# Performance work log

Hardware: AMD Instinct MI355X
Metric: run time of the kernel (lower is better)

## Reference

```python
import jax, jax.numpy as jnp
import numpy as np

EPS = 1e-5

def knn_idx(x, k):
    # x: (B,C,N). Returns (B,N,k) indices of k nearest neighbors (by L2).
    inner = -2.0 * jnp.einsum('bcn,bcm->bnm', x, x)          # (B,N,N)
    xx = jnp.sum(x * x, axis=1)                               # (B,N)
    neg_dist = -xx[:, :, None] - inner - xx[:, None, :]       # (B,N,N)
    _, idx = jax.lax.top_k(neg_dist, k)                       # (B,N,k)
    return idx

def get_graph_features(x, k):
    # x: (B,C,N) -> (B,2C,N,k) with channels = concat(neighbor-center, center)
    B, C, N = x.shape
    idx = knn_idx(x, k)                                       # (B,N,k)
    pts = jnp.transpose(x, (0, 2, 1))                         # (B,N,C)
    nbr = jax.vmap(lambda p, i: p[i])(pts, idx)               # (B,N,k,C)
    ctr = jnp.broadcast_to(pts[:, :, None, :], nbr.shape)     # (B,N,k,C)
    feat = jnp.concatenate([nbr - ctr, ctr], axis=-1)         # (B,N,k,2C)
    return jnp.transpose(feat, (0, 3, 1, 2))                  # (B,2C,N,k)

def conv_bn_relu(y, W, gamma, beta):
    # 1x1 conv (pointwise matmul) + train-mode BatchNorm2d + ReLU
    y = jnp.einsum('oc,bcnk->bonk', W, y)
    mean = jnp.mean(y, axis=(0, 2, 3), keepdims=True)
    var = jnp.var(y, axis=(0, 2, 3), keepdims=True)
    yhat = (y - mean) * jax.lax.rsqrt(var + EPS)
    return jax.nn.relu(yhat * gamma[None, :, None, None] + beta[None, :, None, None])

def setup_inputs() -> dict:
    key = jax.random.key(0)
    ks = jax.random.split(key, 16)
    B, N, k, emb = 8, 2048, 20, 512
    x = jax.random.normal(ks[0], (B, 3, N), dtype=jnp.float32)
    def w(kk, o, c):
        return jax.random.normal(kk, (o, c), dtype=jnp.float32) * (1.0 / np.sqrt(c))
    inp = {
        'x': x, 'k': k,
        'W1': w(ks[1], 64, 6),   'W2': w(ks[2], 64, 64),
        'W3': w(ks[3], 128, 64), 'W4': w(ks[4], 256, 128),
        'W5': w(ks[5], emb, 512),
    }
    for i, c in zip(range(1, 6), [64, 64, 128, 256, emb]):
        inp[f'g{i}'] = 1.0 + 0.1 * jax.random.normal(ks[5 + i], (c,), dtype=jnp.float32)
        inp[f'b{i}'] = 0.1 * jax.random.normal(ks[10 + i], (c,), dtype=jnp.float32)
    return inp

def reference(x, W1, W2, W3, W4, W5, g1, b1, g2, b2, g3, b3, g4, b4, g5, b5, k):
    B, C, N = x.shape
    h = get_graph_features(x, k)                  # (B,6,N,k)
    h = conv_bn_relu(h, W1, g1, b1)               # (B,64,N,k)
    x1 = jnp.max(h, axis=-1, keepdims=True)
    h = conv_bn_relu(h, W2, g2, b2)               # (B,64,N,k)
    x2 = jnp.max(h, axis=-1, keepdims=True)
    h = conv_bn_relu(h, W3, g3, b3)               # (B,128,N,k)
    x3 = jnp.max(h, axis=-1, keepdims=True)
    h = conv_bn_relu(h, W4, g4, b4)               # (B,256,N,k)
    x4 = jnp.max(h, axis=-1, keepdims=True)
    cat = jnp.concatenate([x1, x2, x3, x4], axis=1)  # (B,512,N,1)
    out = conv_bn_relu(cat, W5, g5, b5)              # (B,emb,N,1)
    return out.reshape(B, -1, N)
```

## Files before the change

### kernel.cpp

```cpp
#include <hip/hip_runtime.h>
#include <hip/hip_bf16.h>

typedef __hip_bfloat16 bf16;
typedef __attribute__((ext_vector_type(8))) short short8v;
typedef __attribute__((ext_vector_type(4))) float f32x4;
typedef unsigned int uint;
typedef unsigned long long u64;

#define BATCH 8
#define NPTS 2048
#define KNN 20
#define NK (NPTS*KNN)
#define P4 (BATCH*NK)
#define BN_TOT (BATCH*NPTS)

union BU { bf16 h; unsigned short u; };
__device__ __forceinline__ unsigned short f2bf(float f){
    BU bu; bu.h = __float2bfloat16(f); return bu.u;
}
__device__ __forceinline__ float bfu2f(unsigned short u){
    return __uint_as_float(((uint)u) << 16);
}
__device__ __forceinline__ uint fenc(float f){
    uint b = __float_as_uint(f);
    return (b & 0x80000000u) ? ~b : (b | 0x80000000u);
}

__global__ void initK(float* __restrict__ shadow)
{
    int t = blockIdx.x*256 + threadIdx.x;
    if (t < 5*16*1024) shadow[t] = 0.f;
}

__global__ void cvtWS(const float* __restrict__ src, short* __restrict__ dst, int Cin)
{
    int t = blockIdx.x*256 + threadIdx.x;
    int co = t / Cin, ci = t - co*Cin;
    dst[(size_t)co*Cin + (ci ^ ((co & 7) << 3))] = (short)f2bf(src[t]);
}

__global__ __launch_bounds__(512)
void knn_kernel(const float* __restrict__ x, int* __restrict__ idx)
{
    #pragma clang fp contract(off)
    __shared__ float4 sp[NPTS];
    const int b  = blockIdx.x / (NPTS/8);
    const int nb = blockIdx.x % (NPTS/8);
    const float* xb = x + (size_t)b*3*NPTS;
    for (int i = threadIdx.x; i < NPTS; i += 512) {
        float y0 = xb[i], y1 = xb[NPTS+i], y2 = xb[2*NPTS+i];
        float4 p; p.x = y0; p.y = y1; p.z = y2;
        p.w = y0*y0 + y1*y1 + y2*y2;
        sp[i] = p;
    }
    __syncthreads();

    const int wave = threadIdx.x >> 6;
    const int lane = threadIdx.x & 63;
    const int n = nb*8 + wave;

    const float4 pn = sp[n];
    const float x0 = pn.x, x1 = pn.y, x2 = pn.z;
    const float xxn = pn.w;

    constexpr int L = 4;
    float bA[L], bB[L]; int iA[L], iB[L];
    #pragma unroll
    for (int i = 0; i < L; ++i) {
        bA[i] = -3e38f; bB[i] = -3e38f; iA[i] = 0x7fffffff; iB[i] = 0x7fffffff;
    }

    #pragma unroll
    for (int t = 0; t < NPTS/128; ++t) {
        int m0 = lane + (2*t)*64, m1 = m0 + 64;
        float4 p0 = sp[m0], p1 = sp[m1];
        float dot0 = x0*p0.x + x1*p0.y + x2*p0.z;
        float v0 = -xxn - (-2.f*dot0) - p0.w;
        float dot1 = x0*p1.x + x1*p1.y + x2*p1.z;
        float v1 = -xxn - (-2.f*dot1) - p1.w;
        int mi0 = m0, mi1 = m1;
        #pragma unroll
        for (int i = 0; i < L; ++i) {
            { bool sw = v0 > bA[i];
              float tv = sw ? bA[i] : v0; int ti = sw ? iA[i] : mi0;
              bA[i] = sw ? v0 : bA[i]; iA[i] = sw ? mi0 : iA[i]; v0 = tv; mi0 = ti; }
            { bool sw = v1 > bB[i];
              float tv = sw ? bB[i] : v1; int ti = sw ? iB[i] : mi1;
              bB[i] = sw ? v1 : bB[i]; iB[i] = sw ? mi1 : iB[i]; v1 = tv; mi1 = ti; }
        }
    }

    u64 kA[L], kB[L];
    #pragma unroll
    for (int i = 0; i < L; ++i) {
        kA[i] = ((u64)fenc(bA[i]) << 32) | (uint)(~iA[i]);
        kB[i] = ((u64)fenc(bB[i]) << 32) | (uint)(~iB[i]);
    }

    size_t obase = ((size_t)b*NPTS + n)*KNN;
    int popA = 0, popB = 0;
    #pragma unroll 1
    for (int s = 0; s < KNN; ++s) {
        bool useA = kA[0] >= kB[0];
        u64 my = useA ? kA[0] : kB[0];
        u64 g = my;
        #pragma unroll
        for (int off = 1; off < 64; off <<= 1) {
            u64 o = __shfl_xor(g, off);
            g = (o > g) ? o : g;
        }
        if (lane == 0) idx[obase + s] = (int)(~(uint)g);
        bool win = (my == g);
        bool pA = win && useA, pB = win && !useA;
        #pragma unroll
        for (int i = 0; i < L-1; ++i) {
            kA[i] = pA ? kA[i+1] : kA[i];
            kB[i] = pB ? kB[i+1] : kB[i];
        }
        kA[L-1] = pA ? 0ULL : kA[L-1];
        kB[L-1] = pB ? 0ULL : kB[L-1];
        popA += pA; popB += pB;
    }

    if (__any((popA >= L) || (popB >= L))) {
        float B[KNN]; int BI[KNN];
        #pragma unroll
        for (int i = 0; i < KNN; ++i) { B[i] = -3e38f; BI[i] = 0x7fffffff; }
        #pragma unroll 1
        for (int j = 0; j < NPTS/64; ++j) {
            int m = lane + j*64;
            float4 p = sp[m];
            float dot = x0*p.x + x1*p.y + x2*p.z;
            float v = -xxn - (-2.f*dot) - p.w;
            int mi = m;
            #pragma unroll
            for (int i = 0; i < KNN; ++i) {
                bool sw = v > B[i];
                float tv = sw ? B[i]  : v;
                int   ti = sw ? BI[i] : mi;
                B[i]  = sw ? v  : B[i];
                BI[i] = sw ? mi : BI[i];
                v = tv; mi = ti;
            }
        }
        #pragma unroll 1
        for (int s = 0; s < KNN; ++s) {
            float mv = B[0]; int mi = BI[0];
            #pragma unroll
            for (int off = 1; off < 64; off <<= 1) {
                float ov = __shfl_xor(mv, off);
                int   oi = __shfl_xor(mi, off);
                if (ov > mv || (ov == mv && oi < mi)) { mv = ov; mi = oi; }
            }
            bool win = (B[0] == mv) && (BI[0] == mi);
            #pragma unroll
            for (int i = 0; i < KNN-1; ++i) {
                B[i]  = win ? B[i+1]  : B[i];
                BI[i] = win ? BI[i+1] : BI[i];
            }
            B[KNN-1]  = win ? -3e38f     : B[KNN-1];
            BI[KNN-1] = win ? 0x7fffffff : BI[KNN-1];
            if (lane == 0) idx[obase + s] = mi;
        }
    }
}

__global__ void conv1T(const float* __restrict__ x, const int* __restrict__ idx,
                       const float* __restrict__ W1, bf16* __restrict__ h1)
{
    int p = blockIdx.x*256 + threadIdx.x;
    int b = p / NK;
    int r = p - b*NK;
    int n = r / KNN;
    int j = idx[p];
    const float* xb = x + (size_t)b*3*NPTS;
    float c0 = xb[n], c1 = xb[NPTS+n], c2 = xb[2*NPTS+n];
    float d0 = xb[j]-c0, d1 = xb[NPTS+j]-c1, d2 = xb[2*NPTS+j]-c2;
    uint4* outp = reinterpret_cast<uint4*>(reinterpret_cast<unsigned short*>(h1) + (size_t)p*64);
    #pragma unroll
    for (int ch = 0; ch < 8; ++ch) {
        uint u[4];
        #pragma unroll
        for (int q = 0; q < 4; ++q) {
            const float* wa = W1 + (ch*8 + q*2)*6;
            float a0 = wa[0]*d0 + wa[1]*d1 + wa[2]*d2 + wa[3]*c0 + wa[4]*c1 + wa[5]*c2;
            const float* wb = wa + 6;
            float a1 = wb[0]*d0 + wb[1]*d1 + wb[2]*d2 + wb[3]*c0 + wb[4]*c1 + wb[5]*c2;
            u[q] = (uint)f2bf(a0) | ((uint)f2bf(a1) << 16);
        }
        outp[ch] = make_uint4(u[0], u[1], u[2], u[3]);
    }
}

__global__ void statsT64(const bf16* __restrict__ h, float* __restrict__ shadow)
{
    __shared__ float ls[4][64], lq[4][64];
    int t = threadIdx.x;
    int c = t & 63, grp = t >> 6;
    const unsigned short* hp = reinterpret_cast<const unsigned short*>(h);
    size_t base = (size_t)blockIdx.x*1024;
    float s = 0.f, q = 0.f;
    for (int it = 0; it < 256; ++it) {
        size_t br = base + grp + (size_t)it*4;
        float v = bfu2f(hp[br*64 + c]);
        s += v; q += v*v;
    }
    ls[grp][c] = s; lq[grp][c] = q;
    __syncthreads();
    if (t < 64) {
        float S = ls[0][t]+ls[1][t]+ls[2][t]+ls[3][t];
        float Q = lq[0][t]+lq[1][t]+lq[2][t]+lq[3][t];
        float* sh = shadow + (size_t)(blockIdx.x & 15)*1024;
        atomicAdd(&sh[t], S);
        atomicAdd(&sh[512 + t], Q);
    }
}

__global__ void fin_kernel(const float* __restrict__ shadow,
                           const float* __restrict__ gamma, const float* __restrict__ beta,
                           float* __restrict__ scbiF, int C, float invCnt)
{
    for (int c = threadIdx.x; c < C; c += 256) {
        float s = 0.f, q = 0.f;
        #pragma unroll
        for (int i = 0; i < 16; ++i) { s += shadow[i*1024 + c]; q += shadow[i*1024 + 512 + c]; }
        float m = s*invCnt;
        float var = q*invCnt - m*m;
        float rs = rsqrtf(var + 1e-5f);
        float sc = rs * gamma[c];
        float bi = fmaf(-m, sc, beta[c]);
        scbiF[2*c] = sc; scbiF[2*c+1] = bi;
    }
}

template<int Cout, int Cin, int M, int POOL, int NSPLIT, int KTILE, int BT, int PF>
__global__ __launch_bounds__(BT)
void gemmT(const short* __restrict__ Wb, const bf16* __restrict__ in,
           bf16* __restrict__ outT, float* __restrict__ shadow,
           float* __restrict__ pmax, float* __restrict__ pmin)
{
    constexpr int CSPL = Cout/NSPLIT;
    constexpr int NT   = CSPL/16;
    constexpr int ROWS = (BT/64)*16*M;
    constexpr int KSTOT = Cin/32;
    constexpr int KPT   = KTILE/32;
    constexpr int NTILE = Cin/KTILE;
    constexpr size_t WB = (size_t)CSPL*KTILE*2;
    constexpr size_t PB = POOL ? (size_t)2*ROWS*17*4 : 0;
    constexpr size_t SB = WB > PB ? WB : PB;

    __shared__ __align__(16) char smem[SB];
    short* WsmS = reinterpret_cast<short*>(smem);
    float* poolF = reinterpret_cast<float*>(smem);

    const int tid  = threadIdx.x;
    const int lane = tid & 63;
    const int g = lane >> 4, mr = lane & 15;
    const int wid = tid >> 6;
    const int rowBlk = blockIdx.x*ROWS;
    const int rowW   = rowBlk + wid*(16*M);
    const int ntBase = blockIdx.y*CSPL;
    const short* inS = reinterpret_cast<const short*>(in);

    f32x4 acc[M][NT];
    #pragma unroll
    for (int m = 0; m < M; ++m)
    #pragma unroll
    for (int i = 0; i < NT; ++i) acc[m][i] = (f32x4){0.f,0.f,0.f,0.f};

    short8v a[M], anext[M];
    if (PF) {
        #pragma unroll
        for (int m = 0; m < M; ++m)
            a[m] = *reinterpret_cast<const short8v*>(inS + (size_t)(rowW + m*16 + mr)*Cin + 8*g);
    }

    #pragma unroll 1
    for (int kt = 0; kt < NTILE; ++kt) {
        if (kt) __syncthreads();
        {
            const int ktBase = kt*KTILE;
            for (int f8 = tid; f8 < CSPL*KTILE/8; f8 += BT) {
                int f = f8*8;
                int row = f / KTILE, col = f - row*KTILE;
                short8v v = *reinterpret_cast<const short8v*>(
                    Wb + (size_t)(ntBase + row)*Cin + ktBase + col);
                *reinterpret_cast<short8v*>(WsmS + f) = v;
            }
        }
        __syncthreads();

        #pragma unroll
        for (int ksl = 0; ksl < KPT; ++ksl) {
            const int ksg = kt*KPT + ksl;
            const int k0 = ksg*32 + 8*g;
            if (!PF) {
                #pragma unroll
                for (int m = 0; m < M; ++m)
                    a[m] = *reinterpret_cast<const short8v*>(inS + (size_t)(rowW + m*16 + mr)*Cin + k0);
            } else if (ksg + 1 < KSTOT) {
                #pragma unroll
                for (int m = 0; m < M; ++m)
                    anext[m] = *reinterpret_cast<const short8v*>(inS + (size_t)(rowW + m*16 + mr)*Cin + k0 + 32);
            }
            const int kx = ksl*32 + 8*g;
            #pragma unroll
            for (int nt = 0; nt < NT; ++nt) {
                const int brow = nt*16 + mr;
                short8v bfr = *reinterpret_cast<const short8v*>(
                    WsmS + brow*KTILE + (kx ^ ((mr & 7) << 3)));
                #pragma unroll
                for (int m = 0; m < M; ++m)
                    acc[m][nt] = __builtin_amdgcn_mfma_f32_16x16x32_bf16(a[m], bfr, acc[m][nt], 0, 0, 0);
            }
            if (PF) {
                #pragma unroll
                for (int m = 0; m < M; ++m) a[m] = anext[m];
            }
        }
    }

    float* sh = shadow + (size_t)((blockIdx.x ^ blockIdx.y) & 15)*1024;
    #pragma unroll
    for (int nt = 0; nt < NT; ++nt) {
        float s = 0.f, q = 0.f;
        #pragma unroll
        for (int m = 0; m < M; ++m)
        #pragma unroll
        for (int j = 0; j < 4; ++j) { float v = acc[m][nt][j]; s += v; q += v*v; }
        s += __shfl_xor(s, 16); s += __shfl_xor(s, 32);
        q += __shfl_xor(q, 16); q += __shfl_xor(q, 32);
        if (g == 0) {
            atomicAdd(&sh[ntBase + nt*16 + mr], s);
            atomicAdd(&sh[512 + ntBase + nt*16 + mr], q);
        }
    }

    if (!POOL) {
        #pragma unroll
        for (int m = 0; m < M; ++m)
        #pragma unroll
        for (int nt = 0; nt < NT; ++nt)
        #pragma unroll
        for (int j = 0; j < 4; ++j) {
            size_t row = (size_t)rowW + m*16 + g*4 + j;
            outT[row*Cout + ntBase + nt*16 + mr] = __float2bfloat16(acc[m][nt][j]);
        }
    } else {
        __syncthreads();
        #pragma unroll
        for (int np = 0; np < NT/2; ++np) {
            #pragma unroll
            for (int hh = 0; hh < 2; ++hh) {
                #pragma unroll
                for (int m = 0; m < M; ++m)
                #pragma unroll
                for (int j = 0; j < 4; ++j) {
                    int row = wid*(16*M) + m*16 + g*4 + j;
                    poolF[hh*(ROWS*17) + row*17 + mr] = acc[m][np*2+hh][j];
                }
            }
            __syncthreads();
            if (tid < 2*(ROWS/KNN)*16) {
                int hh = tid >> 7;
                int gg = (tid >> 4) & 7;
                int cc = tid & 15;
                float mx = -3e38f, mn = 3e38f;
                #pragma unroll
                for (int kk = 0; kk < KNN; ++kk) {
                    float v = poolF[hh*(ROWS*17) + (gg*KNN + kk)*17 + cc];
                    mx = fmaxf(mx, v); mn = fminf(mn, v);
                }
                int grp = rowBlk/KNN + gg;
                int c = ntBase + (np*2 + hh)*16 + cc;
                pmax[(size_t)grp*256 + c] = mx;
                pmin[(size_t)grp*256 + c] = mn;
            }
            __syncthreads();
        }
    }
}

template<int C>
__global__ void maxpoolT(bf16* __restrict__ h, const float* __restrict__ scbiF,
                         bf16* __restrict__ catT, int coff)
{
    constexpr int PB = 256/C;
    int t = threadIdx.x;
    int c = t & (C-1);
    int bn = blockIdx.x*PB + t/C;
    float sc = scbiF[2*c], bi = scbiF[2*c+1];
    unsigned short* src = reinterpret_cast<unsigned short*>(h) + (size_t)bn*KNN*C + c;
    float best = 0.f;
    #pragma unroll
    for (int kk = 0; kk < KNN; ++kk) {
        float a = fmaxf(fmaf(bfu2f(src[kk*C]), sc, bi), 0.f);
        src[kk*C] = f2bf(a);
        best = fmaxf(best, a);
    }
    catT[(size_t)bn*512 + coff + c] = __float2bfloat16(best);
}

__global__ void cat4T(const float* __restrict__ pmax, const float* __restrict__ pmin,
                      const float* __restrict__ scbiF, const float* __restrict__ g4,
                      bf16* __restrict__ catT)
{
    int t = blockIdx.x*256 + threadIdx.x;
    int c = t & 255, bn = t >> 8;
    float sc = scbiF[2*c], bi = scbiF[2*c+1];
    float v = (g4[c] >= 0.f) ? pmax[t] : pmin[t];
    catT[(size_t)bn*512 + 256 + c] = __float2bfloat16(fmaxf(fmaf(v, sc, bi), 0.f));
}

__global__ void finalT(const bf16* __restrict__ h5, const float* __restrict__ scbiF,
                       float* __restrict__ out)
{
    __shared__ float ls[64][65];
    int t = threadIdx.x;
    int b = blockIdx.z, n0 = blockIdx.x*64, c0 = blockIdx.y*64;
    int j = t & 63, i0 = t >> 6;
    float sc = scbiF[2*(c0+j)], bi = scbiF[2*(c0+j)+1];
    const unsigned short* hp = reinterpret_cast<const unsigned short*>(h5);
    for (int it = 0; it < 16; ++it) {
        int i = i0 + it*4;
        float v = bfu2f(hp[((size_t)(b*NPTS + n0 + i))*512 + c0 + j]);
        ls[i][j] = fmaxf(fmaf(v, sc, bi), 0.f);
    }
    __syncthreads();
    for (int it = 0; it < 16; ++it) {
        int cr = i0 + it*4;
        out[((size_t)b*512 + c0 + cr)*NPTS + n0 + j] = ls[j][cr];
    }
}

extern "C" void kernel_launch(void* const* d_in, const int* in_sizes, int n_in,
                              void* d_out, int out_size, void* d_ws, size_t ws_size,
                              hipStream_t stream)
{
    const float* x  = (const float*)d_in[0];
    const float* W1 = (const float*)d_in[2];
    const float* W2 = (const float*)d_in[3];
    const float* W3 = (const float*)d_in[4];
    const float* W4 = (const float*)d_in[5];
    const float* W5 = (const float*)d_in[6];
    const float* g1 = (const float*)d_in[7];  const float* b1 = (const float*)d_in[8];
    const float* g2 = (const float*)d_in[9];  const float* b2 = (const float*)d_in[10];
    const float* g3 = (const float*)d_in[11]; const float* b3 = (const float*)d_in[12];
    const float* g4 = (const float*)d_in[13]; const float* b4 = (const float*)d_in[14];
    const float* g5 = (const float*)d_in[15]; const float* b5 = (const float*)d_in[16];
    float* out = (float*)d_out;

    char* w = (char*)d_ws;
    int*   idx    = (int*)w;
    float* scbiF  = (float*)(w + 1323008);
    float* shadow = (float*)(w + 1343488);
    short* Wb     = (short*)(w + 1671168);
    bf16*  h1     = (bf16*)(w + 2285568);
    float* pmax   = (float*)h1;
    float* pmin   = pmax + (size_t)BN_TOT*256;
    bf16*  h2     = (bf16*)(w + 44228608);
    bf16*  h5     = h2;
    bf16*  h3     = (bf16*)(w + 86171648);
    bf16*  catT   = (bf16*)(w + 170057728);

    short* Wb2 = Wb, *Wb3 = Wb + 4096, *Wb4 = Wb + 12288, *Wb5 = Wb + 45056;
    float* sh1 = shadow, *sh2 = shadow + 16384, *sh3 = shadow + 2*16384,
         * sh4 = shadow + 3*16384, *sh5 = shadow + 4*16384;

    initK<<<320, 256, 0, stream>>>(shadow);
    cvtWS<<<16,   256, 0, stream>>>(W2, Wb2, 64);
    cvtWS<<<32,   256, 0, stream>>>(W3, Wb3, 64);
    cvtWS<<<128,  256, 0, stream>>>(W4, Wb4, 128);
    cvtWS<<<1024, 256, 0, stream>>>(W5, Wb5, 512);

    knn_kernel<<<BATCH*NPTS/8, 512, 0, stream>>>(x, idx);
    conv1T<<<P4/256, 256, 0, stream>>>(x, idx, W1, h1);

    statsT64<<<320, 256, 0, stream>>>(h1, sh1);
    fin_kernel<<<1, 256, 0, stream>>>(sh1, g1, b1, scbiF, 64, 1.f/P4);
    maxpoolT<64><<<BN_TOT/4, 256, 0, stream>>>(h1, scbiF, catT, 0);

    gemmT<64,64,2,0,1,64,256,1><<<dim3(P4/128,1), 256, 0, stream>>>(
        Wb2, h1, h2, sh2, nullptr, nullptr);
    fin_kernel<<<1, 256, 0, stream>>>(sh2, g2, b2, scbiF + 1024, 64, 1.f/P4);
    maxpoolT<64><<<BN_TOT/4, 256, 0, stream>>>(h2, scbiF + 1024, catT, 64);

    gemmT<128,64,2,0,1,64,256,1><<<dim3(P4/128,1), 256, 0, stream>>>(
        Wb3, h2, h3, sh3, nullptr, nullptr);
    fin_kernel<<<1, 256, 0, stream>>>(sh3, g3, b3, scbiF + 2048, 128, 1.f/P4);
    maxpoolT<128><<<BN_TOT/2, 256, 0, stream>>>(h3, scbiF + 2048, catT, 128);

    gemmT<256,128,2,1,2,128,320,1><<<dim3(P4/160,2), 320, 0, stream>>>(
        Wb4, h3, nullptr, sh4, pmax, pmin);
    fin_kernel<<<1, 256, 0, stream>>>(sh4, g4, b4, scbiF + 3072, 256, 1.f/P4);
    cat4T<<<BN_TOT, 256, 0, stream>>>(pmax, pmin, scbiF + 3072, g4, catT);

    gemmT<512,512,2,0,4,128,256,1><<<dim3(BN_TOT/128,4), 256, 0, stream>>>(
        Wb5, catT, h5, sh5, nullptr, nullptr);
    fin_kernel<<<1, 256, 0, stream>>>(sh5, g5, b5, scbiF + 4096, 512, 1.f/BN_TOT);
    finalT<<<dim3(NPTS/64, 8, BATCH), 256, 0, stream>>>(h5, scbiF + 4096, out);
}
```

Baseline: 375.2 us.

## Load GEMM weight fragments directly from global memory instead of LDS staging

The GEMM kernel no longer stages weight tiles in swizzled shared memory behind barriers. Each lane now loads its B fragments straight from global memory, and small-Cin layers preload all A and B fragments into registers before issuing the MFMAs. The weight conversion kernel drops the XOR swizzle to match. The kNN loop also gains register double-buffering of the LDS point reads. The change removes LDS traffic and __syncthreads, at the cost of redundant global/L2 weight loads per wave and higher register pressure.

```diff
diff --git a/kernel.cpp b/kernel.cpp
--- a/kernel.cpp
+++ b/kernel.cpp
@@ -32,11 +32,10 @@
     if (t < 5*16*1024) shadow[t] = 0.f;
 }
 
-__global__ void cvtWS(const float* __restrict__ src, short* __restrict__ dst, int Cin)
+__global__ void cvtW(const float* __restrict__ src, short* __restrict__ dst, int n)
 {
     int t = blockIdx.x*256 + threadIdx.x;
-    int co = t / Cin, ci = t - co*Cin;
-    dst[(size_t)co*Cin + (ci ^ ((co & 7) << 3))] = (short)f2bf(src[t]);
+    if (t < n) dst[t] = (short)f2bf(src[t]);
 }
 
 __global__ __launch_bounds__(512)
@@ -70,14 +69,19 @@
         bA[i] = -3e38f; bB[i] = -3e38f; iA[i] = 0x7fffffff; iB[i] = 0x7fffffff;
     }
 
+    float4 c0 = sp[lane], c1 = sp[lane + 64];
     #pragma unroll
     for (int t = 0; t < NPTS/128; ++t) {
+        float4 n0, n1;
+        if (t + 1 < NPTS/128) {
+            n0 = sp[lane + (2*t+2)*64];
+            n1 = sp[lane + (2*t+3)*64];
+        }
         int m0 = lane + (2*t)*64, m1 = m0 + 64;
-        float4 p0 = sp[m0], p1 = sp[m1];
-        float dot0 = x0*p0.x + x1*p0.y + x2*p0.z;
-        float v0 = -xxn - (-2.f*dot0) - p0.w;
-        float dot1 = x0*p1.x + x1*p1.y + x2*p1.z;
-        float v1 = -xxn - (-2.f*dot1) - p1.w;
+        float dot0 = x0*c0.x + x1*c0.y + x2*c0.z;
+        float v0 = -xxn - (-2.f*dot0) - c0.w;
+        float dot1 = x0*c1.x + x1*c1.y + x2*c1.z;
+        float v1 = -xxn - (-2.f*dot1) - c1.w;
         int mi0 = m0, mi1 = m1;
         #pragma unroll
         for (int i = 0; i < L; ++i) {
@@ -88,6 +92,7 @@
               float tv = sw ? bB[i] : v1; int ti = sw ? iB[i] : mi1;
               bB[i] = sw ? v1 : bB[i]; iB[i] = sw ? mi1 : iB[i]; v1 = tv; mi1 = ti; }
         }
+        c0 = n0; c1 = n1;
     }
 
     u64 kA[L], kB[L];
@@ -233,25 +238,19 @@
     }
 }
 
-template<int Cout, int Cin, int M, int POOL, int NSPLIT, int KTILE, int BT, int PF>
+template<int Cout, int Cin, int M, int POOL, int NSPLIT, int BT, int PRB>
 __global__ __launch_bounds__(BT)
-void gemmT(const short* __restrict__ Wb, const bf16* __restrict__ in,
+void gemmR(const short* __restrict__ Wb, const bf16* __restrict__ in,
            bf16* __restrict__ outT, float* __restrict__ shadow,
            float* __restrict__ pmax, float* __restrict__ pmin)
 {
     constexpr int CSPL = Cout/NSPLIT;
     constexpr int NT   = CSPL/16;
+    constexpr int KS   = Cin/32;
     constexpr int ROWS = (BT/64)*16*M;
-    constexpr int KSTOT = Cin/32;
-    constexpr int KPT   = KTILE/32;
-    constexpr int NTILE = Cin/KTILE;
-    constexpr size_t WB = (size_t)CSPL*KTILE*2;
-    constexpr size_t PB = POOL ? (size_t)2*ROWS*17*4 : 0;
-    constexpr size_t SB = WB > PB ? WB : PB;
-
-    __shared__ __align__(16) char smem[SB];
-    short* WsmS = reinterpret_cast<short*>(smem);
-    float* poolF = reinterpret_cast<float*>(smem);
+    constexpr int PFL  = POOL ? 2*ROWS*17 : 4;
+
+    __shared__ __align__(16) float poolF[PFL];
 
     const int tid  = threadIdx.x;
     const int lane = tid & 63;
@@ -268,55 +267,54 @@
     #pragma unroll
     for (int i = 0; i < NT; ++i) acc[m][i] = (f32x4){0.f,0.f,0.f,0.f};
 
-    short8v a[M], anext[M];
-    if (PF) {
+    if (PRB) {
+        short8v Bf[NT*KS], Af[M*KS];
+        #pragma unroll
+        for (int nt = 0; nt < NT; ++nt)
+        #pragma unroll
+        for (int ks = 0; ks < KS; ++ks)
+            Bf[nt*KS+ks] = *reinterpret_cast<const short8v*>(
+                Wb + (size_t)(ntBase + nt*16 + mr)*Cin + ks*32 + 8*g);
+        #pragma unroll
+        for (int m = 0; m < M; ++m)
+        #pragma unroll
+        for (int ks = 0; ks < KS; ++ks)
+            Af[m*KS+ks] = *reinterpret_cast<const short8v*>(
+                inS + (size_t)(rowW + m*16 + mr)*Cin + ks*32 + 8*g);
+        #pragma unroll
+        for (int ks = 0; ks < KS; ++ks)
+        #pragma unroll
+        for (int nt = 0; nt < NT; ++nt)
+        #pragma unroll
+        for (int m = 0; m < M; ++m)
+            acc[m][nt] = __builtin_amdgcn_mfma_f32_16x16x32_bf16(
+                Af[m*KS+ks], Bf[nt*KS+ks], acc[m][nt], 0, 0, 0);
+    } else {
+        short8v a[M], an[M];
         #pragma unroll
         for (int m = 0; m < M; ++m)
             a[m] = *reinterpret_cast<const short8v*>(inS + (size_t)(rowW + m*16 + mr)*Cin + 8*g);
-    }
-
-    #pragma unroll 1
-    for (int kt = 0; kt < NTILE; ++kt) {
-        if (kt) __syncthreads();
-        {
-            const int ktBase = kt*KTILE;
-            for (int f8 = tid; f8 < CSPL*KTILE/8; f8 += BT) {
-                int f = f8*8;
-                int row = f / KTILE, col = f - row*KTILE;
-                short8v v = *reinterpret_cast<const short8v*>(
-                    Wb + (size_t)(ntBase + row)*Cin + ktBase + col);
-                *reinterpret_cast<short8v*>(WsmS + f) = v;
-            }
-        }
-        __syncthreads();
-
-        #pragma unroll
-        for (int ksl = 0; ksl < KPT; ++ksl) {
-            const int ksg = kt*KPT + ksl;
-            const int k0 = ksg*32 + 8*g;
-            if (!PF) {
+        #pragma unroll
+        for (int ks = 0; ks < KS; ++ks) {
+            const int k0 = ks*32 + 8*g;
+            if (ks + 1 < KS) {
                 #pragma unroll
                 for (int m = 0; m < M; ++m)
-                    a[m] = *reinterpret_cast<const short8v*>(inS + (size_t)(rowW + m*16 + mr)*Cin + k0);
-            } else if (ksg + 1 < KSTOT) {
-                #pragma unroll
-                for (int m = 0; m < M; ++m)
-                    anext[m] = *reinterpret_cast<const short8v*>(inS + (size_t)(rowW + m*16 + mr)*Cin + k0 + 32);
-            }
-            const int kx = ksl*32 + 8*g;
-            #pragma unroll
-            for (int nt = 0; nt < NT; ++nt) {
-                const int brow = nt*16 + mr;
-                short8v bfr = *reinterpret_cast<const short8v*>(
-                    WsmS + brow*KTILE + (kx ^ ((mr & 7) << 3)));
-                #pragma unroll
-                for (int m = 0; m < M; ++m)
-                    acc[m][nt] = __builtin_amdgcn_mfma_f32_16x16x32_bf16(a[m], bfr, acc[m][nt], 0, 0, 0);
-            }
-            if (PF) {
-                #pragma unroll
-                for (int m = 0; m < M; ++m) a[m] = anext[m];
-            }
+                    an[m] = *reinterpret_cast<const short8v*>(
+                        inS + (size_t)(rowW + m*16 + mr)*Cin + k0 + 32);
+            }
+            short8v Bf[NT];
+            #pragma unroll
+            for (int nt = 0; nt < NT; ++nt)
+                Bf[nt] = *reinterpret_cast<const short8v*>(
+                    Wb + (size_t)(ntBase + nt*16 + mr)*Cin + k0);
+            #pragma unroll
+            for (int nt = 0; nt < NT; ++nt)
+            #pragma unroll
+            for (int m = 0; m < M; ++m)
+                acc[m][nt] = __builtin_amdgcn_mfma_f32_16x16x32_bf16(a[m], Bf[nt], acc[m][nt], 0, 0, 0);
+            #pragma unroll
+            for (int m = 0; m < M; ++m) a[m] = an[m];
         }
     }
 
@@ -347,7 +345,6 @@
             outT[row*Cout + ntBase + nt*16 + mr] = __float2bfloat16(acc[m][nt][j]);
         }
     } else {
-        __syncthreads();
         #pragma unroll
         for (int np = 0; np < NT/2; ++np) {
             #pragma unroll
@@ -468,10 +465,10 @@
          * sh4 = shadow + 3*16384, *sh5 = shadow + 4*16384;
 
     initK<<<320, 256, 0, stream>>>(shadow);
-    cvtWS<<<16,   256, 0, stream>>>(W2, Wb2, 64);
-    cvtWS<<<32,   256, 0, stream>>>(W3, Wb3, 64);
-    cvtWS<<<128,  256, 0, stream>>>(W4, Wb4, 128);
-    cvtWS<<<1024, 256, 0, stream>>>(W5, Wb5, 512);
+    cvtW<<<16,   256, 0, stream>>>(W2, Wb2, 4096);
+    cvtW<<<32,   256, 0, stream>>>(W3, Wb3, 8192);
+    cvtW<<<128,  256, 0, stream>>>(W4, Wb4, 32768);
+    cvtW<<<1024, 256, 0, stream>>>(W5, Wb5, 262144);
 
     knn_kernel<<<BATCH*NPTS/8, 512, 0, stream>>>(x, idx);
     conv1T<<<P4/256, 256, 0, stream>>>(x, idx, W1, h1);
@@ -480,22 +477,22 @@
     fin_kernel<<<1, 256, 0, stream>>>(sh1, g1, b1, scbiF, 64, 1.f/P4);
     maxpoolT<64><<<BN_TOT/4, 256, 0, stream>>>(h1, scbiF, catT, 0);
 
-    gemmT<64,64,2,0,1,64,256,1><<<dim3(P4/128,1), 256, 0, stream>>>(
+    gemmR<64,64,2,0,1,256,1><<<dim3(P4/128,1), 256, 0, stream>>>(
         Wb2, h1, h2, sh2, nullptr, nullptr);
     fin_kernel<<<1, 256, 0, stream>>>(sh2, g2, b2, scbiF + 1024, 64, 1.f/P4);
     maxpoolT<64><<<BN_TOT/4, 256, 0, stream>>>(h2, scbiF + 1024, catT, 64);
 
-    gemmT<128,64,2,0,1,64,256,1><<<dim3(P4/128,1), 256, 0, stream>>>(
+    gemmR<128,64,2,0,1,256,1><<<dim3(P4/128,1), 256, 0, stream>>>(
         Wb3, h2, h3, sh3, nullptr, nullptr);
     fin_kernel<<<1, 256, 0, stream>>>(sh3, g3, b3, scbiF + 2048, 128, 1.f/P4);
     maxpoolT<128><<<BN_TOT/2, 256, 0, stream>>>(h3, scbiF + 2048, catT, 128);
 
-    gemmT<256,128,2,1,2,128,320,1><<<dim3(P4/160,2), 320, 0, stream>>>(
+    gemmR<256,128,2,1,2,320,0><<<dim3(P4/160,2), 320, 0, stream>>>(
         Wb4, h3, nullptr, sh4, pmax, pmin);
     fin_kernel<<<1, 256, 0, stream>>>(sh4, g4, b4, scbiF + 3072, 256, 1.f/P4);
     cat4T<<<BN_TOT, 256, 0, stream>>>(pmax, pmin, scbiF + 3072, g4, catT);
 
-    gemmT<512,512,2,0,4,128,256,1><<<dim3(BN_TOT/128,4), 256, 0, stream>>>(
+    gemmR<512,512,2,0,4,256,0><<<dim3(BN_TOT/128,4), 256, 0, stream>>>(
         Wb5, catT, h5, sh5, nullptr, nullptr);
     fin_kernel<<<1, 256, 0, stream>>>(sh5, g5, b5, scbiF + 4096, 512, 1.f/BN_TOT);
     finalT<<<dim3(NPTS/64, 8, BATCH), 256, 0, stream>>>(h5, scbiF + 4096, out);
```

New measurement: 456.6 us. 21.7% more time.

## Fuse BN1 statistics into conv1, prefetch KNN LDS loads, widen layer-4 GEMM blocks

Applied to the files above, without the earlier changes.

Computes layer-1 BatchNorm sum and sum-of-squares inside conv1T from an LDS copy of each block's output. This removes the separate statsT64 kernel and its re-read of h1. The KNN scan loop now software-prefetches the next pair of candidate points from LDS. The pooled layer-4 GEMM uses 640-thread blocks covering twice as many rows, with the pool group count generalized. The risks are extra LDS use in conv1T and lower occupancy for the larger GEMM blocks.

```diff
diff --git a/kernel.cpp b/kernel.cpp
--- a/kernel.cpp
+++ b/kernel.cpp
@@ -70,14 +70,19 @@
         bA[i] = -3e38f; bB[i] = -3e38f; iA[i] = 0x7fffffff; iB[i] = 0x7fffffff;
     }
 
+    float4 c0 = sp[lane], c1 = sp[lane + 64];
     #pragma unroll
     for (int t = 0; t < NPTS/128; ++t) {
+        float4 n0, n1;
+        if (t + 1 < NPTS/128) {
+            n0 = sp[lane + (2*t+2)*64];
+            n1 = sp[lane + (2*t+3)*64];
+        }
         int m0 = lane + (2*t)*64, m1 = m0 + 64;
-        float4 p0 = sp[m0], p1 = sp[m1];
-        float dot0 = x0*p0.x + x1*p0.y + x2*p0.z;
-        float v0 = -xxn - (-2.f*dot0) - p0.w;
-        float dot1 = x0*p1.x + x1*p1.y + x2*p1.z;
-        float v1 = -xxn - (-2.f*dot1) - p1.w;
+        float dot0 = x0*c0.x + x1*c0.y + x2*c0.z;
+        float v0 = -xxn - (-2.f*dot0) - c0.w;
+        float dot1 = x0*c1.x + x1*c1.y + x2*c1.z;
+        float v1 = -xxn - (-2.f*dot1) - c1.w;
         int mi0 = m0, mi1 = m1;
         #pragma unroll
         for (int i = 0; i < L; ++i) {
@@ -88,6 +93,7 @@
               float tv = sw ? bB[i] : v1; int ti = sw ? iB[i] : mi1;
               bB[i] = sw ? v1 : bB[i]; iB[i] = sw ? mi1 : iB[i]; v1 = tv; mi1 = ti; }
         }
+        c0 = n0; c1 = n1;
     }
 
     u64 kA[L], kB[L];
@@ -165,10 +171,15 @@
     }
 }
 
-__global__ void conv1T(const float* __restrict__ x, const int* __restrict__ idx,
-                       const float* __restrict__ W1, bf16* __restrict__ h1)
-{
-    int p = blockIdx.x*256 + threadIdx.x;
+__global__ __launch_bounds__(256)
+void conv1T(const float* __restrict__ x, const int* __restrict__ idx,
+            const float* __restrict__ W1, bf16* __restrict__ h1,
+            float* __restrict__ shadow)
+{
+    __shared__ unsigned short lv[256][64];
+    __shared__ float ps[4][64], pq[4][64];
+    const int tid = threadIdx.x;
+    int p = blockIdx.x*256 + tid;
     int b = p / NK;
     int r = p - b*NK;
     int n = r / KNN;
@@ -177,6 +188,7 @@
     float c0 = xb[n], c1 = xb[NPTS+n], c2 = xb[2*NPTS+n];
     float d0 = xb[j]-c0, d1 = xb[NPTS+j]-c1, d2 = xb[2*NPTS+j]-c2;
     uint4* outp = reinterpret_cast<uint4*>(reinterpret_cast<unsigned short*>(h1) + (size_t)p*64);
+    uint4* lrow = reinterpret_cast<uint4*>(lv[tid]);
     #pragma unroll
     for (int ch = 0; ch < 8; ++ch) {
         uint u[4];
@@ -188,31 +200,26 @@
             float a1 = wb[0]*d0 + wb[1]*d1 + wb[2]*d2 + wb[3]*c0 + wb[4]*c1 + wb[5]*c2;
             u[q] = (uint)f2bf(a0) | ((uint)f2bf(a1) << 16);
         }
-        outp[ch] = make_uint4(u[0], u[1], u[2], u[3]);
-    }
-}
-
-__global__ void statsT64(const bf16* __restrict__ h, float* __restrict__ shadow)
-{
-    __shared__ float ls[4][64], lq[4][64];
-    int t = threadIdx.x;
-    int c = t & 63, grp = t >> 6;
-    const unsigned short* hp = reinterpret_cast<const unsigned short*>(h);
-    size_t base = (size_t)blockIdx.x*1024;
+        uint4 val = make_uint4(u[0], u[1], u[2], u[3]);
+        outp[ch] = val;
+        lrow[ch] = val;
+    }
+    __syncthreads();
+    int c = tid & 63, grp = tid >> 6;
     float s = 0.f, q = 0.f;
-    for (int it = 0; it < 256; ++it) {
-        size_t br = base + grp + (size_t)it*4;
-        float v = bfu2f(hp[br*64 + c]);
+    #pragma unroll 8
+    for (int i = 0; i < 64; ++i) {
+        float v = bfu2f(lv[grp*64 + i][c]);
         s += v; q += v*v;
     }
-    ls[grp][c] = s; lq[grp][c] = q;
+    ps[grp][c] = s; pq[grp][c] = q;
     __syncthreads();
-    if (t < 64) {
-        float S = ls[0][t]+ls[1][t]+ls[2][t]+ls[3][t];
-        float Q = lq[0][t]+lq[1][t]+lq[2][t]+lq[3][t];
+    if (tid < 64) {
+        float S = ps[0][tid]+ps[1][tid]+ps[2][tid]+ps[3][tid];
+        float Q = pq[0][tid]+pq[1][tid]+pq[2][tid]+pq[3][tid];
         float* sh = shadow + (size_t)(blockIdx.x & 15)*1024;
-        atomicAdd(&sh[t], S);
-        atomicAdd(&sh[512 + t], Q);
+        atomicAdd(&sh[tid], S);
+        atomicAdd(&sh[512 + tid], Q);
     }
 }
 
@@ -245,6 +252,7 @@
     constexpr int KSTOT = Cin/32;
     constexpr int KPT   = KTILE/32;
     constexpr int NTILE = Cin/KTILE;
+    constexpr int NG    = POOL ? ROWS/KNN : 1;
     constexpr size_t WB = (size_t)CSPL*KTILE*2;
     constexpr size_t PB = POOL ? (size_t)2*ROWS*17*4 : 0;
     constexpr size_t SB = WB > PB ? WB : PB;
@@ -361,9 +369,9 @@
                 }
             }
             __syncthreads();
-            if (tid < 2*(ROWS/KNN)*16) {
-                int hh = tid >> 7;
-                int gg = (tid >> 4) & 7;
+            if (tid < 2*NG*16) {
+                int hh = tid / (NG*16);
+                int gg = (tid >> 4) % NG;
                 int cc = tid & 15;
                 float mx = -3e38f, mn = 3e38f;
                 #pragma unroll
@@ -474,9 +482,8 @@
     cvtWS<<<1024, 256, 0, stream>>>(W5, Wb5, 512);
 
     knn_kernel<<<BATCH*NPTS/8, 512, 0, stream>>>(x, idx);
-    conv1T<<<P4/256, 256, 0, stream>>>(x, idx, W1, h1);
-
-    statsT64<<<320, 256, 0, stream>>>(h1, sh1);
+    conv1T<<<P4/256, 256, 0, stream>>>(x, idx, W1, h1, sh1);
+
     fin_kernel<<<1, 256, 0, stream>>>(sh1, g1, b1, scbiF, 64, 1.f/P4);
     maxpoolT<64><<<BN_TOT/4, 256, 0, stream>>>(h1, scbiF, catT, 0);
 
@@ -490,7 +497,7 @@
     fin_kernel<<<1, 256, 0, stream>>>(sh3, g3, b3, scbiF + 2048, 128, 1.f/P4);
     maxpoolT<128><<<BN_TOT/2, 256, 0, stream>>>(h3, scbiF + 2048, catT, 128);
 
-    gemmT<256,128,2,1,2,128,320,1><<<dim3(P4/160,2), 320, 0, stream>>>(
+    gemmT<256,128,2,1,2,128,640,1><<<dim3(P4/320,2), 640, 0, stream>>>(
         Wb4, h3, nullptr, sh4, pmax, pmin);
     fin_kernel<<<1, 256, 0, stream>>>(sh4, g4, b4, scbiF + 3072, 256, 1.f/P4);
     cat4T<<<BN_TOT, 256, 0, stream>>>(pmax, pmin, scbiF + 3072, g4, catT);
```

Result: faster. 362.5 us (-3.4%).
